# Optimization experiments

Hardware: AMD Instinct MI355X
Metric: run time of the kernel (lower is better)

Reference implementation:

```python
import jax, jax.numpy as jnp
import numpy as np

B, T, C, H = 4, 2048, 1024, 16
HS = C // H  # head dim = 64
EPS = 1e-5


def _layernorm(h, w, b):
    m = jnp.mean(h, axis=-1, keepdims=True)
    v = jnp.mean(jnp.square(h - m), axis=-1, keepdims=True)
    return (h - m) * jax.lax.rsqrt(v + EPS) * w + b


def _quantize_int8(t):
    # per-tensor absmax int8 quantization, matching the torch code
    absmax = jnp.max(jnp.abs(t))
    scale = jnp.where(absmax > 0, absmax / 127.0, jnp.float32(1.0))
    q = jnp.clip(jnp.round(t / scale), -127, 127).astype(jnp.int8)
    return q, scale


def setup_inputs() -> dict:
    key = jax.random.key(0)
    ks = jax.random.split(key, 8)
    w = lambda k, shape: (jax.random.normal(k, shape, jnp.float32) * 0.02)
    return {
        "x": jax.random.normal(ks[0], (B, T, C), jnp.float32),
        "ln1_w": jnp.ones((C,), jnp.float32),
        "ln1_b": jnp.zeros((C,), jnp.float32),
        "W_qkv": w(ks[1], (C, 3 * C)),
        "b_qkv": jnp.zeros((3 * C,), jnp.float32),
        "W_o": w(ks[2], (C, C)),
        "b_o": jnp.zeros((C,), jnp.float32),
        "ln2_w": jnp.ones((C,), jnp.float32),
        "ln2_b": jnp.zeros((C,), jnp.float32),
        "W_fc": w(ks[3], (C, 4 * C)),
        "b_fc": jnp.zeros((4 * C,), jnp.float32),
        "W_pr": w(ks[4], (4 * C, C)),
        "b_pr": jnp.zeros((C,), jnp.float32),
    }


def reference(x, ln1_w, ln1_b, W_qkv, b_qkv, W_o, b_o, ln2_w, ln2_b, W_fc, b_fc, W_pr, b_pr):
    # ---- attention (prefill, cache-owner, kv_cache_quant=True, use_cache=True) ----
    h = _layernorm(x, ln1_w, ln1_b)
    qkv = h @ W_qkv + b_qkv                       # (B,T,3C)
    q, k, v = jnp.split(qkv, 3, axis=-1)
    q = q.reshape(B, T, H, HS).transpose(0, 2, 1, 3)  # (B,H,T,hs)
    k = k.reshape(B, T, H, HS).transpose(0, 2, 1, 3)
    v = v.reshape(B, T, H, HS).transpose(0, 2, 1, 3)

    # quantized `present` cache (returned, not used for attention in prefill path)
    k_quant, k_scale = _quantize_int8(k)
    v_quant, v_scale = _quantize_int8(v)

    # causal SDPA (dropout=0)
    att = jnp.einsum("bhqd,bhkd->bhqk", q, k) * (1.0 / np.sqrt(HS))
    causal = jnp.tril(jnp.ones((T, T), bool))
    att = jnp.where(causal[None, None], att, jnp.float32(-jnp.inf))
    att = jax.nn.softmax(att, axis=-1)
    y = jnp.einsum("bhqk,bhkd->bhqd", att, v)
    y = y.transpose(0, 2, 1, 3).reshape(B, T, C)
    y = y @ W_o + b_o
    x = x + y

    # ---- MLP ----
    h2 = _layernorm(x, ln2_w, ln2_b)
    h2 = jax.nn.gelu(h2 @ W_fc + b_fc, approximate=False)
    x = x + (h2 @ W_pr + b_pr)

    return x, k_quant, k_scale, v_quant, v_scale
```

## Files before the change

### kernel.cpp

```cpp
#include <hip/hip_runtime.h>
#include <cmath>

typedef __bf16 bf16;
typedef float f32x4 __attribute__((ext_vector_type(4)));
typedef __bf16 bf16x4 __attribute__((ext_vector_type(4)));
typedef __bf16 bf16x8 __attribute__((ext_vector_type(8)));

#define DEVI __device__ __forceinline__

constexpr int Bn = 4, Tn = 2048, Cn = 1024, Hn = 16, HSn = 64;
constexpr int C3n = 3 * Cn;
constexpr int BTn = Bn * Tn;

constexpr size_t OFF_WT_QKV = 0;
constexpr size_t OFF_WT_O   = 6291456;
constexpr size_t OFF_WT_FC  = 8388608;
constexpr size_t OFF_WT_PR  = 16777216;
constexpr size_t OFF_H      = 25165824;
constexpr size_t OFF_Y      = 41943040;
constexpr size_t OFF_X1     = 58720256;
constexpr size_t OFF_AMAX   = 92274688;
constexpr size_t OFF_QKV    = 92274944;
constexpr size_t OFF_G      = OFF_QKV;

constexpr size_t OUT_X  = 0;
constexpr size_t OUT_KQ = 8388608;
constexpr size_t OUT_KS = 16777216;
constexpr size_t OUT_VQ = 16777217;
constexpr size_t OUT_VS = 25165825;

DEVI void g2l16(const void* g, void* l) {
  __builtin_amdgcn_global_load_lds(
      (__attribute__((address_space(1))) void*)g,
      (__attribute__((address_space(3))) void*)l, 16, 0, 0);
}

DEVI float gelu_f(float x) {
  const float ax = fabsf(x) * 0.7071067811865476f;
  const float t = 1.0f / (1.0f + 0.3275911f * ax);
  const float p = t * (0.254829592f + t * (-0.284496736f +
                  t * (1.421413741f + t * (-1.453152027f + t * 1.061405429f))));
  float er = 1.0f - p * __expf(-ax * ax);
  er = (x < 0.0f) ? -er : er;
  return 0.5f * x * (1.0f + er);
}

__global__ __launch_bounds__(256) void k_transpose(const float* __restrict__ W,
                                                   bf16* __restrict__ Wt,
                                                   int K, int N) {
  __shared__ float tile[32][33];
  const int n0 = blockIdx.x * 32, k0 = blockIdx.y * 32;
  const int tx = threadIdx.x, ty = threadIdx.y;
#pragma unroll
  for (int i = 0; i < 4; ++i) {
    int k = k0 + ty + i * 8;
    tile[ty + i * 8][tx] = W[(size_t)k * N + (n0 + tx)];
  }
  __syncthreads();
#pragma unroll
  for (int i = 0; i < 4; ++i) {
    int n = n0 + ty + i * 8;
    Wt[(size_t)n * K + (k0 + tx)] = (bf16)tile[tx][ty + i * 8];
  }
}

__global__ __launch_bounds__(256) void k_ln(const float* __restrict__ x,
                                            const float* __restrict__ g,
                                            const float* __restrict__ b,
                                            bf16* __restrict__ out) {
  __shared__ float red[8];
  const int row = blockIdx.x, tid = threadIdx.x;
  const int lane = tid & 63, wv = tid >> 6;
  f32x4 v = ((const f32x4*)(x + (size_t)row * Cn))[tid];

  float s = v[0] + v[1] + v[2] + v[3];
  s += __shfl_down(s, 32); s += __shfl_down(s, 16); s += __shfl_down(s, 8);
  s += __shfl_down(s, 4);  s += __shfl_down(s, 2);  s += __shfl_down(s, 1);
  if (!lane) red[wv] = s;
  __syncthreads();
  const float mean = (red[0] + red[1] + red[2] + red[3]) * (1.0f / 1024.0f);
  __syncthreads();

  f32x4 d = v - mean;
  float s2 = d[0]*d[0] + d[1]*d[1] + d[2]*d[2] + d[3]*d[3];
  s2 += __shfl_down(s2, 32); s2 += __shfl_down(s2, 16); s2 += __shfl_down(s2, 8);
  s2 += __shfl_down(s2, 4);  s2 += __shfl_down(s2, 2);  s2 += __shfl_down(s2, 1);
  if (!lane) red[wv] = s2;
  __syncthreads();
  const float var = (red[0] + red[1] + red[2] + red[3]) * (1.0f / 1024.0f);
  const float inv = rsqrtf(var + 1e-5f);

  f32x4 gw = ((const f32x4*)g)[tid];
  f32x4 bb = ((const f32x4*)b)[tid];
  bf16x4 o;
#pragma unroll
  for (int j = 0; j < 4; ++j) o[j] = (bf16)(d[j] * inv * gw[j] + bb[j]);
  *(bf16x4*)(out + (size_t)row * Cn + tid * 4) = o;
}

template <bool BF16OUT, bool RES, bool GELU, bool AMAX>
__global__ __launch_bounds__(256) void k_gemm(const bf16* __restrict__ A,
                                              const bf16* __restrict__ Bt,
                                              const float* __restrict__ bias,
                                              const float* __restrict__ res,
                                              void* __restrict__ Cout,
                                              unsigned int* __restrict__ amax,
                                              int M, int N, int K) {
  __shared__ bf16 As[128 * 64];
  __shared__ bf16 Bs[128 * 64];
  __shared__ float redA[4];
  const int tid = threadIdx.x;
  const int lane = tid & 63;
  const int w = tid >> 6;
  const int wm = w & 1, wn = w >> 1;
  const int l15 = lane & 15, quad = lane >> 4;
  const int m0 = blockIdx.x * 128, n0 = blockIdx.y * 128;

  const int srow = lane >> 3;
  const int sch = ((lane & 7) ^ srow) * 8;
  const bf16* aBase = A  + (size_t)(m0 + srow) * K + sch;
  const bf16* bBase = Bt + (size_t)(n0 + srow) * K + sch;

  f32x4 acc[4][4] = {};
  const int kIters = K >> 6;
  for (int kt = 0; kt < kIters; ++kt) {
    const size_t kOff = (size_t)kt * 64;
#pragma unroll
    for (int j = 0; j < 4; ++j) {
      const int g = w + 4 * j;
      g2l16(aBase + (size_t)(8 * g) * K + kOff, As + g * 512);
      g2l16(bBase + (size_t)(8 * g) * K + kOff, Bs + g * 512);
    }
    __builtin_amdgcn_s_waitcnt(0);
    __syncthreads();

#pragma unroll
    for (int kk = 0; kk < 2; ++kk) {
      bf16x8 af[4], bv[4];
#pragma unroll
      for (int mt = 0; mt < 4; ++mt) {
        const int m = wm * 64 + mt * 16 + l15;
        const int c = ((kk * 4 + quad) ^ (l15 & 7)) * 8;
        af[mt] = *(const bf16x8*)(As + m * 64 + c);
      }
#pragma unroll
      for (int nt = 0; nt < 4; ++nt) {
        const int n = wn * 64 + nt * 16 + l15;
        const int c = ((kk * 4 + quad) ^ (l15 & 7)) * 8;
        bv[nt] = *(const bf16x8*)(Bs + n * 64 + c);
      }
#pragma unroll
      for (int mt = 0; mt < 4; ++mt)
#pragma unroll
        for (int nt = 0; nt < 4; ++nt)
          acc[mt][nt] = __builtin_amdgcn_mfma_f32_16x16x32_bf16(af[mt], bv[nt], acc[mt][nt], 0, 0, 0);
    }
    __syncthreads();
  }

  const int colB = n0 + wn * 64 + l15;
  const int rowB = m0 + wm * 64 + (quad << 2);
  float lm = 0.0f;
#pragma unroll
  for (int mt = 0; mt < 4; ++mt) {
#pragma unroll
    for (int nt = 0; nt < 4; ++nt) {
      const int col = colB + nt * 16;
      const float bval = bias[col];
#pragma unroll
      for (int r = 0; r < 4; ++r) {
        const int row = rowB + mt * 16 + r;
        float val = acc[mt][nt][r] + bval;
        if (GELU) val = gelu_f(val);
        if (RES)  val += res[(size_t)row * N + col];
        if (AMAX) lm = fmaxf(lm, fabsf(val));
        if (BF16OUT) ((bf16*)Cout)[(size_t)row * N + col] = (bf16)val;
        else         ((float*)Cout)[(size_t)row * N + col] = val;
      }
    }
  }

  if (AMAX) {
    const int cls = n0 >> 10;
    if (cls > 0) {
      lm = fmaxf(lm, __shfl_xor(lm, 1));
      lm = fmaxf(lm, __shfl_xor(lm, 2));
      lm = fmaxf(lm, __shfl_xor(lm, 4));
      lm = fmaxf(lm, __shfl_xor(lm, 8));
      lm = fmaxf(lm, __shfl_xor(lm, 16));
      lm = fmaxf(lm, __shfl_xor(lm, 32));
      if (!lane) redA[w] = lm;
      __syncthreads();
      if (tid == 0) {
        const float m4 = fmaxf(fmaxf(redA[0], redA[1]), fmaxf(redA[2], redA[3]));
        atomicMax(amax + (cls - 1), __float_as_uint(m4));
      }
    }
  }
}

__global__ __launch_bounds__(256) void k_init(unsigned int* amax) {
  if (threadIdx.x < 2) amax[threadIdx.x] = 0u;
}

__global__ __launch_bounds__(256) void k_quant(const bf16* __restrict__ qkv,
                                               const unsigned int* __restrict__ amax,
                                               float* __restrict__ out) {
  const float ka = __uint_as_float(amax[0]);
  const float va = __uint_as_float(amax[1]);
  const float ks = ka > 0.0f ? ka / 127.0f : 1.0f;
  const float vs = va > 0.0f ? va / 127.0f : 1.0f;
  if (blockIdx.x == 0 && threadIdx.x == 0) { out[OUT_KS] = ks; out[OUT_VS] = vs; }
  const float kinv = 1.0f / ks, vinv = 1.0f / vs;
  const size_t nchunks = 1048576;
  const size_t stride = (size_t)gridDim.x * blockDim.x;
  for (size_t ci = (size_t)blockIdx.x * blockDim.x + threadIdx.x; ci < nchunks; ci += stride) {
    const int d0 = (int)(ci & 7) * 8;
    const int t  = (int)(ci >> 3) & 2047;
    const int h  = (int)(ci >> 14) & 15;
    const int b  = (int)(ci >> 18);
    const size_t src = ((size_t)(b * Tn + t)) * C3n + h * HSn + d0;
    bf16x8 k8 = *(const bf16x8*)(qkv + src + Cn);
    bf16x8 v8 = *(const bf16x8*)(qkv + src + 2 * Cn);
    float kq[8], vq[8];
#pragma unroll
    for (int j = 0; j < 8; ++j) {
      kq[j] = fminf(fmaxf(rintf((float)k8[j] * kinv), -127.0f), 127.0f);
      vq[j] = fminf(fmaxf(rintf((float)v8[j] * vinv), -127.0f), 127.0f);
    }
    const size_t oi = ci * 8;
    f32x4 a0 = {kq[0], kq[1], kq[2], kq[3]};
    f32x4 a1 = {kq[4], kq[5], kq[6], kq[7]};
    *(f32x4*)(out + OUT_KQ + oi)     = a0;
    *(f32x4*)(out + OUT_KQ + oi + 4) = a1;
    float* vdst = out + OUT_VQ + oi;
#pragma unroll
    for (int j = 0; j < 8; ++j) vdst[j] = vq[j];
  }
}

__global__ __launch_bounds__(256, 3) void k_attn(const bf16* __restrict__ qkv,
                                                 bf16* __restrict__ y) {
  __shared__ bf16 Ks[2][64 * 64];
  __shared__ bf16 Vt[2][64 * 64];
  __shared__ bf16 Pt[4][2][16 * 64];

  const int tid = threadIdx.x;
  const int lane = tid & 63;
  const int w = tid >> 6;
  const int quad = lane >> 4;
  const int l15 = lane & 15;

  const int bh = blockIdx.x;
  const int qt = 15 - (int)blockIdx.y;
  const int b = bh >> 4, h = bh & 15;
  const int q0 = qt * 128;
  const int ktMax = 2 * qt + 1;

  const bf16* qkv_b = qkv + (size_t)b * Tn * C3n + h * HSn;
  const bf16* kbase = qkv_b + Cn;
  const bf16* vbase = qkv_b + 2 * Cn;

  const int srow = lane >> 3;
  const int schunk = ((lane & 7) ^ srow) * 8;

  const bf16* q0p = qkv_b + (size_t)(q0 + 16 * w + l15) * C3n;
  const bf16* q1p = q0p + (size_t)64 * C3n;
  bf16x8 qf[2][2];
  qf[0][0] = *(const bf16x8*)(q0p + quad * 8);
  qf[0][1] = *(const bf16x8*)(q0p + 32 + quad * 8);
  qf[1][0] = *(const bf16x8*)(q1p + quad * 8);
  qf[1][1] = *(const bf16x8*)(q1p + 32 + quad * 8);

  g2l16(kbase + (size_t)(8 * w + srow) * C3n + schunk, (bf16*)Ks[0] + w * 512);
  g2l16(kbase + (size_t)(8 * (w + 4) + srow) * C3n + schunk, (bf16*)Ks[0] + (w + 4) * 512);
  bf16x8 v0 = *(const bf16x8*)(vbase + (size_t)lane * C3n + w * 8);
  bf16x8 v1 = *(const bf16x8*)(vbase + (size_t)lane * C3n + (w + 4) * 8);
  __builtin_amdgcn_s_waitcnt(0);
#pragma unroll
  for (int j = 0; j < 8; ++j) {
    Vt[0][(w * 8 + j) * 64 + ((srow ^ j) << 3) + (lane & 7)] = v0[j];
    Vt[0][((w + 4) * 8 + j) * 64 + ((srow ^ j) << 3) + (lane & 7)] = v1[j];
  }
  __syncthreads();

  f32x4 Od[2][4] = {};
  float m_i[2] = {-INFINITY, -INFINITY};
  float l_i[2] = {0.0f, 0.0f};

  for (int kt = 0; kt <= ktMax; ++kt) {
    const int bsel = kt & 1;

    bf16x8 nv0, nv1;
    if (kt < ktMax) {
      const int kv1 = (kt + 1) * 64;
      g2l16(kbase + (size_t)(kv1 + 8 * w + srow) * C3n + schunk,
            (bf16*)Ks[bsel ^ 1] + w * 512);
      g2l16(kbase + (size_t)(kv1 + 8 * (w + 4) + srow) * C3n + schunk,
            (bf16*)Ks[bsel ^ 1] + (w + 4) * 512);
      nv0 = *(const bf16x8*)(vbase + (size_t)(kv1 + lane) * C3n + w * 8);
      nv1 = *(const bf16x8*)(vbase + (size_t)(kv1 + lane) * C3n + (w + 4) * 8);
    }

    const bf16* KsB = Ks[bsel];
    f32x4 S0[4] = {}, S1[4] = {};
#pragma unroll
    for (int ks = 0; ks < 2; ++ks)
#pragma unroll
      for (int nt = 0; nt < 4; ++nt) {
        const int rn = nt * 16 + l15;
        const int c = ((ks * 4 + quad) ^ (l15 & 7)) * 8;
        bf16x8 kf = *(const bf16x8*)(KsB + rn * 64 + c);
        S0[nt] = __builtin_amdgcn_mfma_f32_16x16x32_bf16(kf, qf[0][ks], S0[nt], 0, 0, 0);
        S1[nt] = __builtin_amdgcn_mfma_f32_16x16x32_bf16(kf, qf[1][ks], S1[nt], 0, 0, 0);
      }

    const int qloc = 16 * w + l15;
    const int th[2] = { kt < 2 * qt ? 64 : (kt == 2 * qt ? qloc : -1),
                        kt < ktMax ? 64 : qloc };
    f32x4* Sg[2] = {S0, S1};
#pragma unroll
    for (int g = 0; g < 2; ++g) {
      float s[4][4];
      float mx = -INFINITY;
#pragma unroll
      for (int nt = 0; nt < 4; ++nt)
#pragma unroll
        for (int r = 0; r < 4; ++r) {
          float v = Sg[g][nt][r] * 0.125f;
          if (nt * 16 + quad * 4 + r > th[g]) v = -INFINITY;
          s[nt][r] = v;
          mx = fmaxf(mx, v);
        }
      mx = fmaxf(mx, __shfl_xor(mx, 16));
      mx = fmaxf(mx, __shfl_xor(mx, 32));
      const float mn = fmaxf(m_i[g], mx);
      const float al = __expf(m_i[g] - mn);
      m_i[g] = mn;
      float rsum = 0.0f;
      bf16x4 pk[4];
#pragma unroll
      for (int nt = 0; nt < 4; ++nt)
#pragma unroll
        for (int r = 0; r < 4; ++r) {
          const float p = __expf(s[nt][r] - mn);
          rsum += p;
          pk[nt][r] = (bf16)p;
        }
      rsum += __shfl_xor(rsum, 16);
      rsum += __shfl_xor(rsum, 32);
      l_i[g] = l_i[g] * al + rsum;
#pragma unroll
      for (int dt = 0; dt < 4; ++dt) Od[g][dt] *= al;
#pragma unroll
      for (int nt = 0; nt < 4; ++nt) {
        const int phys = (nt * 2 + (quad >> 1)) ^ (l15 & 7);
        *(bf16x4*)(&Pt[w][g][0] + l15 * 64 + phys * 8 + (quad & 1) * 4) = pk[nt];
      }
    }

    const bf16* VtB = Vt[bsel];
#pragma unroll
    for (int ks2 = 0; ks2 < 2; ++ks2) {
      const int pc = ((ks2 * 4 + quad) ^ (l15 & 7)) * 8;
      bf16x8 pf0 = *(const bf16x8*)(&Pt[w][0][0] + l15 * 64 + pc);
      bf16x8 pf1 = *(const bf16x8*)(&Pt[w][1][0] + l15 * 64 + pc);
#pragma unroll
      for (int dt = 0; dt < 4; ++dt) {
        const int d = dt * 16 + l15;
        bf16x8 vf = *(const bf16x8*)(VtB + d * 64 + pc);
        Od[0][dt] = __builtin_amdgcn_mfma_f32_16x16x32_bf16(vf, pf0, Od[0][dt], 0, 0, 0);
        Od[1][dt] = __builtin_amdgcn_mfma_f32_16x16x32_bf16(vf, pf1, Od[1][dt], 0, 0, 0);
      }
    }

    if (kt < ktMax) {
      __builtin_amdgcn_s_waitcnt(0);
#pragma unroll
      for (int j = 0; j < 8; ++j) {
        Vt[bsel ^ 1][(w * 8 + j) * 64 + ((srow ^ j) << 3) + (lane & 7)] = nv0[j];
        Vt[bsel ^ 1][((w + 4) * 8 + j) * 64 + ((srow ^ j) << 3) + (lane & 7)] = nv1[j];
      }
      __syncthreads();
    }
  }

#pragma unroll
  for (int g = 0; g < 2; ++g) {
    const float invl = 1.0f / l_i[g];
    const size_t yb = ((size_t)b * Tn + q0 + g * 64 + 16 * w + l15) * Cn + h * HSn;
#pragma unroll
    for (int dt = 0; dt < 4; ++dt) {
      bf16x4 o;
#pragma unroll
      for (int r = 0; r < 4; ++r) o[r] = (bf16)(Od[g][dt][r] * invl);
      *(bf16x4*)(y + yb + dt * 16 + quad * 4) = o;
    }
  }
}

extern "C" void kernel_launch(void* const* d_in, const int* in_sizes, int n_in,
                              void* d_out, int out_size, void* d_ws, size_t ws_size,
                              hipStream_t stream) {
  const float* x     = (const float*)d_in[0];
  const float* ln1w  = (const float*)d_in[1];
  const float* ln1b  = (const float*)d_in[2];
  const float* Wqkv  = (const float*)d_in[3];
  const float* bqkv  = (const float*)d_in[4];
  const float* Wo    = (const float*)d_in[5];
  const float* bo    = (const float*)d_in[6];
  const float* ln2w  = (const float*)d_in[7];
  const float* ln2b  = (const float*)d_in[8];
  const float* Wfc   = (const float*)d_in[9];
  const float* bfc   = (const float*)d_in[10];
  const float* Wpr   = (const float*)d_in[11];
  const float* bpr   = (const float*)d_in[12];

  char* ws = (char*)d_ws;
  bf16*  Wt_qkv = (bf16*)(ws + OFF_WT_QKV);
  bf16*  Wt_o   = (bf16*)(ws + OFF_WT_O);
  bf16*  Wt_fc  = (bf16*)(ws + OFF_WT_FC);
  bf16*  Wt_pr  = (bf16*)(ws + OFF_WT_PR);
  bf16*  h      = (bf16*)(ws + OFF_H);
  bf16*  ybf    = (bf16*)(ws + OFF_Y);
  float* x1     = (float*)(ws + OFF_X1);
  unsigned int* amax = (unsigned int*)(ws + OFF_AMAX);
  bf16*  qkvbf  = (bf16*)(ws + OFF_QKV);
  bf16*  g      = (bf16*)(ws + OFF_G);
  float* out    = (float*)d_out;

  const dim3 tb(32, 8);
  k_transpose<<<dim3(96, 32),  tb, 0, stream>>>(Wqkv, Wt_qkv, 1024, 3072);
  k_transpose<<<dim3(32, 32),  tb, 0, stream>>>(Wo,   Wt_o,   1024, 1024);
  k_transpose<<<dim3(128, 32), tb, 0, stream>>>(Wfc,  Wt_fc,  1024, 4096);
  k_transpose<<<dim3(32, 128), tb, 0, stream>>>(Wpr,  Wt_pr,  4096, 1024);
  k_init<<<1, 64, 0, stream>>>(amax);

  k_ln<<<BTn, 256, 0, stream>>>(x, ln1w, ln1b, h);
  k_gemm<true, false, false, true><<<dim3(64, 24), 256, 0, stream>>>(h, Wt_qkv, bqkv, nullptr, qkvbf, amax, 8192, 3072, 1024);
  k_quant<<<2048, 256, 0, stream>>>(qkvbf, amax, out);
  k_attn<<<dim3(64, 16), 256, 0, stream>>>(qkvbf, ybf);
  k_gemm<false, true, false, false><<<dim3(64, 8), 256, 0, stream>>>(ybf, Wt_o, bo, x, x1, nullptr, 8192, 1024, 1024);
  k_ln<<<BTn, 256, 0, stream>>>(x1, ln2w, ln2b, h);
  k_gemm<true, false, true, false><<<dim3(64, 32), 256, 0, stream>>>(h, Wt_fc, bfc, nullptr, g, nullptr, 8192, 4096, 1024);
  k_gemm<false, true, false, false><<<dim3(64, 8), 256, 0, stream>>>(g, Wt_pr, bpr, x1, out, nullptr, 8192, 1024, 4096);
}
```

Baseline: 579.2 us.

## Add 256x256 pipelined 512-thread GEMM for QKV and FC projections

Adds a new bf16 MFMA GEMM kernel with 256x256 tiles, 8 waves, and double-buffered LDS staged via direct global-to-LDS loads. It interleaves half-tile prefetches with MFMA quarters using manual vmcnt waits, barriers and s_setprio. The QKV and FC projections now use it, aiming for more data reuse per tile and better overlap of loads with compute. The cost is heavy register pressure from 32 accumulator tiles and hand-tuned waitcnt counts that must match the issued loads exactly.

```diff
diff --git a/kernel.cpp b/kernel.cpp
--- a/kernel.cpp
+++ b/kernel.cpp
@@ -194,6 +194,175 @@
       if (tid == 0) {
         const float m4 = fmaxf(fmaxf(redA[0], redA[1]), fmaxf(redA[2], redA[3]));
         atomicMax(amax + (cls - 1), __float_as_uint(m4));
+      }
+    }
+  }
+}
+
+#define VMBAR(N) asm volatile("s_waitcnt vmcnt(" #N ")\n\ts_barrier" ::: "memory")
+#define BARW()   asm volatile("s_barrier" ::: "memory")
+#define MEMFENCE() asm volatile("" ::: "memory")
+
+DEVI void stage_half(const bf16* __restrict__ G, int ldk, int row0, int k0,
+                     bf16* dst, int w, int lane) {
+  const int srow = lane >> 3;
+  const int sch = ((lane & 7) ^ srow) * 8;
+  const bf16* src = G + (size_t)(row0 + srow) * ldk + k0 + sch;
+#pragma unroll
+  for (int i = 0; i < 2; ++i) {
+    const int g = 2 * w + i;
+    g2l16(src + (size_t)(8 * g) * ldk, dst + g * 512);
+  }
+}
+
+template <int Q>
+DEVI void read_a(const bf16* AsB, int wm, int l15, int quad, bf16x8 (&af)[2][2]) {
+#pragma unroll
+  for (int r = 0; r < 2; ++r)
+#pragma unroll
+    for (int kk = 0; kk < 2; ++kk) {
+      const int row = wm * 128 + (2 * Q + r) * 16 + l15;
+      const int c = ((kk * 4 + quad) ^ (l15 & 7)) * 8;
+      af[r][kk] = *(const bf16x8*)(AsB + row * 64 + c);
+    }
+}
+
+DEVI void read_b(const bf16* BsB, int wn, int l15, int quad, bf16x8 (&bv)[4][2]) {
+#pragma unroll
+  for (int nt = 0; nt < 4; ++nt)
+#pragma unroll
+    for (int kk = 0; kk < 2; ++kk) {
+      const int row = wn * 64 + nt * 16 + l15;
+      const int c = ((kk * 4 + quad) ^ (l15 & 7)) * 8;
+      bv[nt][kk] = *(const bf16x8*)(BsB + row * 64 + c);
+    }
+}
+
+template <int Q>
+DEVI void mfma_q(const bf16x8 (&af)[2][2], const bf16x8 (&bv)[4][2],
+                 f32x4 (&acc)[8][4]) {
+  __builtin_amdgcn_s_setprio(1);
+#pragma unroll
+  for (int r = 0; r < 2; ++r)
+#pragma unroll
+    for (int nt = 0; nt < 4; ++nt)
+#pragma unroll
+      for (int kk = 0; kk < 2; ++kk)
+        acc[2 * Q + r][nt] = __builtin_amdgcn_mfma_f32_16x16x32_bf16(
+            af[r][kk], bv[nt][kk], acc[2 * Q + r][nt], 0, 0, 0);
+  __builtin_amdgcn_s_setprio(0);
+}
+
+template <int BUF>
+DEVI void tile_body(int kt, int kIters, const bf16* __restrict__ A,
+                    const bf16* __restrict__ Bt, int K, int m0, int n0,
+                    bf16 (*As)[16384], bf16 (*Bs)[16384],
+                    bf16x8 (&bvU)[4][2], bf16x8 (&bvN)[4][2],
+                    f32x4 (&acc)[8][4], int w, int lane) {
+  const int l15 = lane & 15, quad = lane >> 4;
+  const int wm = w >> 2, wn = w & 3;
+  const bf16* AsB = As[BUF];
+  const int kLast = kIters - 1;
+  bf16x8 af[2][2];
+
+  if (kt == kLast)      { VMBAR(0); }
+  else if (kt > 0)      { VMBAR(4); }
+  read_a<0>(AsB, wm, l15, quad, af);
+  if (kt + 1 < kIters) stage_half(A, K, m0 + 0, (kt + 1) * 64, As[BUF ^ 1] + 0, w, lane);
+  mfma_q<0>(af, bvU, acc);
+
+  BARW();
+  read_a<1>(AsB, wm, l15, quad, af);
+  if (kt + 1 < kIters) stage_half(A, K, m0 + 128, (kt + 1) * 64, As[BUF ^ 1] + 8192, w, lane);
+  mfma_q<1>(af, bvU, acc);
+
+  BARW();
+  read_a<2>(AsB, wm, l15, quad, af);
+  if (kt + 2 < kIters) stage_half(Bt, K, n0 + 0, (kt + 2) * 64, Bs[BUF] + 0, w, lane);
+  mfma_q<2>(af, bvU, acc);
+
+  if (kt + 2 < kIters)      { VMBAR(6); }
+  else if (kt + 1 < kIters) { VMBAR(4); }
+  else                      { BARW(); }
+  read_a<3>(AsB, wm, l15, quad, af);
+  if (kt + 1 < kIters) read_b(Bs[BUF ^ 1], wn, l15, quad, bvN);
+  if (kt + 2 < kIters) stage_half(Bt, K, n0 + 128, (kt + 2) * 64, Bs[BUF] + 8192, w, lane);
+  mfma_q<3>(af, bvU, acc);
+}
+
+template <bool GELU, bool AMAX>
+__global__ __launch_bounds__(512, 2) void k_gemm256(const bf16* __restrict__ A,
+                                                    const bf16* __restrict__ Bt,
+                                                    const float* __restrict__ bias,
+                                                    bf16* __restrict__ Cout,
+                                                    unsigned int* __restrict__ amax,
+                                                    int M, int N, int K) {
+  __shared__ bf16 As[2][16384];
+  __shared__ bf16 Bs[2][16384];
+  __shared__ float redA[8];
+  const int tid = threadIdx.x;
+  const int lane = tid & 63, w = tid >> 6;
+  const int wm = w >> 2, wn = w & 3;
+  const int l15 = lane & 15, quad = lane >> 4;
+  const int m0 = blockIdx.x * 256, n0 = blockIdx.y * 256;
+  const int kIters = K >> 6;
+  (void)M;
+
+  stage_half(Bt, K, n0 + 0,   0,  Bs[0] + 0,    w, lane);
+  stage_half(Bt, K, n0 + 128, 0,  Bs[0] + 8192, w, lane);
+  stage_half(A,  K, m0 + 0,   0,  As[0] + 0,    w, lane);
+  stage_half(A,  K, m0 + 128, 0,  As[0] + 8192, w, lane);
+  MEMFENCE();
+  stage_half(Bt, K, n0 + 0,   64, Bs[1] + 0,    w, lane);
+  stage_half(Bt, K, n0 + 128, 64, Bs[1] + 8192, w, lane);
+  VMBAR(4);
+
+  f32x4 acc[8][4] = {};
+  bf16x8 bv0[4][2], bv1[4][2];
+  read_b(Bs[0], wn, l15, quad, bv0);
+
+  const int nPairs = kIters >> 1;
+  for (int p = 0; p < nPairs; ++p) {
+    tile_body<0>(2 * p,     kIters, A, Bt, K, m0, n0, As, Bs, bv0, bv1, acc, w, lane);
+    tile_body<1>(2 * p + 1, kIters, A, Bt, K, m0, n0, As, Bs, bv1, bv0, acc, w, lane);
+  }
+
+  const int colB = n0 + wn * 64 + l15;
+  const int rowB = m0 + wm * 128 + (quad << 2);
+  float lm = 0.0f;
+#pragma unroll
+  for (int mt = 0; mt < 8; ++mt) {
+#pragma unroll
+    for (int nt = 0; nt < 4; ++nt) {
+      const int col = colB + nt * 16;
+      const float bval = bias[col];
+#pragma unroll
+      for (int r = 0; r < 4; ++r) {
+        const int row = rowB + mt * 16 + r;
+        float val = acc[mt][nt][r] + bval;
+        if (GELU) val = gelu_f(val);
+        if (AMAX) lm = fmaxf(lm, fabsf(val));
+        Cout[(size_t)row * N + col] = (bf16)val;
+      }
+    }
+  }
+
+  if (AMAX) {
+    const int cls = n0 >> 10;
+    if (cls > 0) {
+      lm = fmaxf(lm, __shfl_xor(lm, 1));
+      lm = fmaxf(lm, __shfl_xor(lm, 2));
+      lm = fmaxf(lm, __shfl_xor(lm, 4));
+      lm = fmaxf(lm, __shfl_xor(lm, 8));
+      lm = fmaxf(lm, __shfl_xor(lm, 16));
+      lm = fmaxf(lm, __shfl_xor(lm, 32));
+      if (!lane) redA[w] = lm;
+      __syncthreads();
+      if (tid == 0) {
+        float m8 = redA[0];
+#pragma unroll
+        for (int i = 1; i < 8; ++i) m8 = fmaxf(m8, redA[i]);
+        atomicMax(amax + (cls - 1), __float_as_uint(m8));
       }
     }
   }
@@ -437,11 +606,11 @@
   k_init<<<1, 64, 0, stream>>>(amax);
 
   k_ln<<<BTn, 256, 0, stream>>>(x, ln1w, ln1b, h);
-  k_gemm<true, false, false, true><<<dim3(64, 24), 256, 0, stream>>>(h, Wt_qkv, bqkv, nullptr, qkvbf, amax, 8192, 3072, 1024);
+  k_gemm256<false, true><<<dim3(32, 12), 512, 0, stream>>>(h, Wt_qkv, bqkv, qkvbf, amax, 8192, 3072, 1024);
   k_quant<<<2048, 256, 0, stream>>>(qkvbf, amax, out);
   k_attn<<<dim3(64, 16), 256, 0, stream>>>(qkvbf, ybf);
   k_gemm<false, true, false, false><<<dim3(64, 8), 256, 0, stream>>>(ybf, Wt_o, bo, x, x1, nullptr, 8192, 1024, 1024);
   k_ln<<<BTn, 256, 0, stream>>>(x1, ln2w, ln2b, h);
-  k_gemm<true, false, true, false><<<dim3(64, 32), 256, 0, stream>>>(h, Wt_fc, bfc, nullptr, g, nullptr, 8192, 4096, 1024);
+  k_gemm256<true, false><<<dim3(32, 16), 512, 0, stream>>>(h, Wt_fc, bfc, g, nullptr, 8192, 4096, 1024);
   k_gemm<false, true, false, false><<<dim3(64, 8), 256, 0, stream>>>(g, Wt_pr, bpr, x1, out, nullptr, 8192, 1024, 4096);
 }
```

Measured after the change: 571.8 us. No clear change (-1.3%).

## Replace GEMM with 256-wide double-buffered pipelined kernel using 8 waves

Applied to the files above, without the earlier changes.

The 128x128 single-buffered GEMM is replaced by a 512-thread kernel with 256-column (and 128 or 256 row) tiles. The A and B tiles are double-buffered in shared memory, and the prefetch of the next k-slice is interleaved across four MFMA phases, using raw s_barrier and vmcnt waits and raised wave priority during MFMA. The goal is to hide global-load latency and raise reuse per tile for all four projection GEMMs. The cost is more LDS, more registers, fewer blocks for the N=1024 GEMMs, and delicate hand-written synchronisation.

```diff
diff --git a/kernel.cpp b/kernel.cpp
--- a/kernel.cpp
+++ b/kernel.cpp
@@ -98,71 +98,129 @@
   *(bf16x4*)(out + (size_t)row * Cn + tid * 4) = o;
 }
 
-template <bool BF16OUT, bool RES, bool GELU, bool AMAX>
-__global__ __launch_bounds__(256) void k_gemm(const bf16* __restrict__ A,
-                                              const bf16* __restrict__ Bt,
-                                              const float* __restrict__ bias,
-                                              const float* __restrict__ res,
-                                              void* __restrict__ Cout,
-                                              unsigned int* __restrict__ amax,
-                                              int M, int N, int K) {
-  __shared__ bf16 As[128 * 64];
-  __shared__ bf16 Bs[128 * 64];
-  __shared__ float redA[4];
-  const int tid = threadIdx.x;
-  const int lane = tid & 63;
-  const int w = tid >> 6;
-  const int wm = w & 1, wn = w >> 1;
-  const int l15 = lane & 15, quad = lane >> 4;
-  const int m0 = blockIdx.x * 128, n0 = blockIdx.y * 128;
-
+#define VMBAR(N) asm volatile("s_waitcnt vmcnt(" #N ")\n\ts_barrier" ::: "memory")
+#define BARW()   asm volatile("s_barrier" ::: "memory")
+
+DEVI void stage_half(const bf16* __restrict__ G, int ldk, int row0, int k0,
+                     bf16* dst, int w, int lane) {
   const int srow = lane >> 3;
   const int sch = ((lane & 7) ^ srow) * 8;
-  const bf16* aBase = A  + (size_t)(m0 + srow) * K + sch;
-  const bf16* bBase = Bt + (size_t)(n0 + srow) * K + sch;
-
-  f32x4 acc[4][4] = {};
-  const int kIters = K >> 6;
+  const bf16* src = G + (size_t)(row0 + srow) * ldk + k0 + sch;
+#pragma unroll
+  for (int i = 0; i < 2; ++i) {
+    const int g = 2 * w + i;
+    g2l16(src + (size_t)(8 * g) * ldk, dst + g * 512);
+  }
+}
+
+DEVI void read_b(const bf16* BsB, int wn, int l15, int quad, bf16x8 (&bv)[4][2]) {
+#pragma unroll
+  for (int nt = 0; nt < 4; ++nt)
+#pragma unroll
+    for (int kk = 0; kk < 2; ++kk) {
+      const int row = wn * 64 + nt * 16 + l15;
+      const int c = ((kk * 4 + quad) ^ (l15 & 7)) * 8;
+      bv[nt][kk] = *(const bf16x8*)(BsB + row * 64 + c);
+    }
+}
+
+template <int MR, int Q>
+DEVI void read_aq(const bf16* AsB, int wm, int l15, int quad, bf16x8 (&af)[MR][2]) {
+#pragma unroll
+  for (int r = 0; r < MR; ++r)
+#pragma unroll
+    for (int kk = 0; kk < 2; ++kk) {
+      const int row = wm * (MR * 64) + (Q * MR + r) * 16 + l15;
+      const int c = ((kk * 4 + quad) ^ (l15 & 7)) * 8;
+      af[r][kk] = *(const bf16x8*)(AsB + row * 64 + c);
+    }
+}
+
+template <int MR, int MF, int Q>
+DEVI void mfma_q(const bf16x8 (&af)[MR][2], const bf16x8 (&bv)[4][2],
+                 f32x4 (&acc)[MF][4]) {
+  __builtin_amdgcn_s_setprio(1);
+#pragma unroll
+  for (int r = 0; r < MR; ++r)
+#pragma unroll
+    for (int nt = 0; nt < 4; ++nt)
+#pragma unroll
+      for (int kk = 0; kk < 2; ++kk)
+        acc[Q * MR + r][nt] = __builtin_amdgcn_mfma_f32_16x16x32_bf16(
+            af[r][kk], bv[nt][kk], acc[Q * MR + r][nt], 0, 0, 0);
+  __builtin_amdgcn_s_setprio(0);
+}
+
+template <int BM, bool RES, bool GELU, bool AMAX, bool F32OUT>
+__global__ __launch_bounds__(512, 2) void k_gemm256(const bf16* __restrict__ A,
+                                                    const bf16* __restrict__ Bt,
+                                                    const float* __restrict__ bias,
+                                                    const float* __restrict__ res,
+                                                    void* __restrict__ Cout,
+                                                    unsigned int* __restrict__ amax,
+                                                    int M, int N, int K) {
+  constexpr int MR = BM / 128;
+  constexpr int MF = BM / 32;
+  __shared__ bf16 As[2][BM * 64];
+  __shared__ bf16 Bs[2][256 * 64];
+  __shared__ float redA[8];
+  const int tid = threadIdx.x;
+  const int lane = tid & 63, w = tid >> 6;
+  const int wm = w >> 2, wn = w & 3;
+  const int l15 = lane & 15, quad = lane >> 4;
+  const int m0 = blockIdx.x * BM, n0 = blockIdx.y * 256;
+  const int kIters = K >> 6, kLast = kIters - 1;
+  (void)M;
+
+#pragma unroll
+  for (int hA = 0; hA < MR; ++hA)
+    stage_half(A, K, m0 + 128 * hA, 0, As[0] + 8192 * hA, w, lane);
+  stage_half(Bt, K, n0 + 0,   0,  Bs[0] + 0,    w, lane);
+  stage_half(Bt, K, n0 + 128, 0,  Bs[0] + 8192, w, lane);
+  stage_half(Bt, K, n0 + 0,   64, Bs[1] + 0,    w, lane);
+  stage_half(Bt, K, n0 + 128, 64, Bs[1] + 8192, w, lane);
+
+  f32x4 acc[MF][4] = {};
+
   for (int kt = 0; kt < kIters; ++kt) {
-    const size_t kOff = (size_t)kt * 64;
-#pragma unroll
-    for (int j = 0; j < 4; ++j) {
-      const int g = w + 4 * j;
-      g2l16(aBase + (size_t)(8 * g) * K + kOff, As + g * 512);
-      g2l16(bBase + (size_t)(8 * g) * K + kOff, Bs + g * 512);
-    }
-    __builtin_amdgcn_s_waitcnt(0);
-    __syncthreads();
-
-#pragma unroll
-    for (int kk = 0; kk < 2; ++kk) {
-      bf16x8 af[4], bv[4];
-#pragma unroll
-      for (int mt = 0; mt < 4; ++mt) {
-        const int m = wm * 64 + mt * 16 + l15;
-        const int c = ((kk * 4 + quad) ^ (l15 & 7)) * 8;
-        af[mt] = *(const bf16x8*)(As + m * 64 + c);
-      }
-#pragma unroll
-      for (int nt = 0; nt < 4; ++nt) {
-        const int n = wn * 64 + nt * 16 + l15;
-        const int c = ((kk * 4 + quad) ^ (l15 & 7)) * 8;
-        bv[nt] = *(const bf16x8*)(Bs + n * 64 + c);
-      }
-#pragma unroll
-      for (int mt = 0; mt < 4; ++mt)
-#pragma unroll
-        for (int nt = 0; nt < 4; ++nt)
-          acc[mt][nt] = __builtin_amdgcn_mfma_f32_16x16x32_bf16(af[mt], bv[nt], acc[mt][nt], 0, 0, 0);
-    }
-    __syncthreads();
+    const bf16* AsB = As[kt & 1];
+    const bf16* BsB = Bs[kt & 1];
+    bf16* AsN = As[(kt & 1) ^ 1];
+    bf16* BsC = Bs[kt & 1];
+    const bool stA = (kt + 1 < kIters);
+    const bool stB = (kt + 2 < kIters);
+    bf16x8 bv[4][2];
+    bf16x8 af[MR][2];
+
+    if (kt == kLast) { VMBAR(0); } else { VMBAR(4); }
+    read_b(BsB, wn, l15, quad, bv);
+    read_aq<MR, 0>(AsB, wm, l15, quad, af);
+    if (stA) stage_half(A, K, m0 + 0, (kt + 1) * 64, AsN + 0, w, lane);
+    mfma_q<MR, MF, 0>(af, bv, acc);
+
+    BARW();
+    read_aq<MR, 1>(AsB, wm, l15, quad, af);
+    if constexpr (BM == 256) {
+      if (stA) stage_half(A, K, m0 + 128, (kt + 1) * 64, AsN + 8192, w, lane);
+    }
+    mfma_q<MR, MF, 1>(af, bv, acc);
+
+    BARW();
+    read_aq<MR, 2>(AsB, wm, l15, quad, af);
+    if (stB) stage_half(Bt, K, n0 + 0, (kt + 2) * 64, BsC + 0, w, lane);
+    mfma_q<MR, MF, 2>(af, bv, acc);
+
+    BARW();
+    read_aq<MR, 3>(AsB, wm, l15, quad, af);
+    if (stB) stage_half(Bt, K, n0 + 128, (kt + 2) * 64, BsC + 8192, w, lane);
+    mfma_q<MR, MF, 3>(af, bv, acc);
   }
 
   const int colB = n0 + wn * 64 + l15;
-  const int rowB = m0 + wm * 64 + (quad << 2);
+  const int rowB = m0 + wm * (BM / 2) + (quad << 2);
   float lm = 0.0f;
 #pragma unroll
-  for (int mt = 0; mt < 4; ++mt) {
+  for (int mt = 0; mt < MF; ++mt) {
 #pragma unroll
     for (int nt = 0; nt < 4; ++nt) {
       const int col = colB + nt * 16;
@@ -174,8 +232,8 @@
         if (GELU) val = gelu_f(val);
         if (RES)  val += res[(size_t)row * N + col];
         if (AMAX) lm = fmaxf(lm, fabsf(val));
-        if (BF16OUT) ((bf16*)Cout)[(size_t)row * N + col] = (bf16)val;
-        else         ((float*)Cout)[(size_t)row * N + col] = val;
+        if (F32OUT) ((float*)Cout)[(size_t)row * N + col] = val;
+        else        ((bf16*)Cout)[(size_t)row * N + col] = (bf16)val;
       }
     }
   }
@@ -192,8 +250,10 @@
       if (!lane) redA[w] = lm;
       __syncthreads();
       if (tid == 0) {
-        const float m4 = fmaxf(fmaxf(redA[0], redA[1]), fmaxf(redA[2], redA[3]));
-        atomicMax(amax + (cls - 1), __float_as_uint(m4));
+        float m8 = redA[0];
+#pragma unroll
+        for (int i = 1; i < 8; ++i) m8 = fmaxf(m8, redA[i]);
+        atomicMax(amax + (cls - 1), __float_as_uint(m8));
       }
     }
   }
@@ -437,11 +497,15 @@
   k_init<<<1, 64, 0, stream>>>(amax);
 
   k_ln<<<BTn, 256, 0, stream>>>(x, ln1w, ln1b, h);
-  k_gemm<true, false, false, true><<<dim3(64, 24), 256, 0, stream>>>(h, Wt_qkv, bqkv, nullptr, qkvbf, amax, 8192, 3072, 1024);
+  k_gemm256<256, false, false, true, false><<<dim3(32, 12), 512, 0, stream>>>(
+      h, Wt_qkv, bqkv, nullptr, qkvbf, amax, 8192, 3072, 1024);
   k_quant<<<2048, 256, 0, stream>>>(qkvbf, amax, out);
   k_attn<<<dim3(64, 16), 256, 0, stream>>>(qkvbf, ybf);
-  k_gemm<false, true, false, false><<<dim3(64, 8), 256, 0, stream>>>(ybf, Wt_o, bo, x, x1, nullptr, 8192, 1024, 1024);
+  k_gemm256<128, true, false, false, true><<<dim3(64, 4), 512, 0, stream>>>(
+      ybf, Wt_o, bo, x, x1, nullptr, 8192, 1024, 1024);
   k_ln<<<BTn, 256, 0, stream>>>(x1, ln2w, ln2b, h);
-  k_gemm<true, false, true, false><<<dim3(64, 32), 256, 0, stream>>>(h, Wt_fc, bfc, nullptr, g, nullptr, 8192, 4096, 1024);
-  k_gemm<false, true, false, false><<<dim3(64, 8), 256, 0, stream>>>(g, Wt_pr, bpr, x1, out, nullptr, 8192, 1024, 4096);
-}
+  k_gemm256<256, false, true, false, false><<<dim3(32, 16), 512, 0, stream>>>(
+      h, Wt_fc, bfc, nullptr, g, nullptr, 8192, 4096, 1024);
+  k_gemm256<128, true, false, false, true><<<dim3(64, 4), 512, 0, stream>>>(
+      g, Wt_pr, bpr, x1, out, nullptr, 8192, 1024, 4096);
+}
```

After: 546.5 us. -5.6%, faster.
